# Kernel tuning notes

Measured on AMD Instinct MI355X. Metric: run time of the kernel, lower is better.

The kernel has to match this reference:

```python
import jax, jax.numpy as jnp
import numpy as np

B, C, H, W = 2, 64, 256, 256
SIZE, STRIDE = 8, 4
NUMS = (H - SIZE) // STRIDE + 1          # 63 patches per axis
L = NUMS * NUMS                           # 3969 patches
K2 = SIZE * SIZE                          # 64 pixels per patch
EPS = 1e-05
TABLE = (2 * NUMS - 1) * (2 * NUMS - 1)   # relative-position bias table size


def _unfold_idx():
    # linear pixel index for each (kernel-offset k, patch l): [K2, L]
    i0 = np.arange(NUMS) * STRIDE
    j0 = np.arange(NUMS) * STRIDE
    kh = np.arange(SIZE)
    kw = np.arange(SIZE)
    r = kh[:, None, None, None] + i0[None, None, :, None]   # [S,1,N,1]
    c = kw[None, :, None, None] + j0[None, None, None, :]   # [1,S,1,N]
    return (r * W + c).reshape(K2, L)


def _rel_pos_index():
    ch = np.arange(NUMS)
    cw = np.arange(NUMS)
    coords = np.stack(np.meshgrid(ch, cw, indexing='ij'))   # [2,N,N]
    cf = coords.reshape(2, -1)                               # [2,L]
    rc = (cf[:, :, None] - cf[:, None, :]).transpose(1, 2, 0).astype(np.int64)
    rc[:, :, 0] += NUMS - 1
    rc[:, :, 1] += NUMS - 1
    rc[:, :, 0] *= 2 * NUMS - 1
    return rc.sum(-1)                                        # [L,L]


_IDX_NP = _unfold_idx()
_IDX = jnp.asarray(_IDX_NP)
_RPI = jnp.asarray(_rel_pos_index())
_count_np = np.zeros(H * W, np.float32)
np.add.at(_count_np, _IDX_NP.ravel(), 1.0)
_COUNT = jnp.asarray(_count_np.reshape(1, 1, H, W))


def setup_inputs() -> dict:
    key = jax.random.key(0)
    ks = jax.random.split(key, 9)
    x = jax.random.normal(ks[0], (B, C, H, W), dtype=jnp.float32)
    mask = jnp.round(jax.random.uniform(ks[1], (B, 1, H, W), dtype=jnp.float32))
    fg_gamma = 0.1 * jax.random.normal(ks[2], (C,), dtype=jnp.float32)
    fg_beta = 0.1 * jax.random.normal(ks[3], (C,), dtype=jnp.float32)
    bg_gamma = 0.1 * jax.random.normal(ks[4], (C,), dtype=jnp.float32)
    bg_beta = 0.1 * jax.random.normal(ks[5], (C,), dtype=jnp.float32)
    w_fore = 0.02 * jax.random.normal(ks[6], (C, C, K2), dtype=jnp.float32)
    w_back = 0.02 * jax.random.normal(ks[7], (C, C, K2), dtype=jnp.float32)
    rpb_table = 0.02 * jax.random.normal(ks[8], (TABLE,), dtype=jnp.float32)
    return {"x": x, "mask": mask, "fg_gamma": fg_gamma, "fg_beta": fg_beta,
            "bg_gamma": bg_gamma, "bg_beta": bg_beta,
            "w_fore": w_fore, "w_back": w_back, "rpb_table": rpb_table}


def _unfold(t):
    # [B,Ct,H,W] -> [B,Ct,L,K2]  (gather patch pixels)
    b, ct = t.shape[0], t.shape[1]
    return t.reshape(b, ct, H * W)[:, :, _IDX].transpose(0, 1, 3, 2)


def _patch_mean_std(region, m):
    # region [B,Ct,L,K2], m [B,1,L,K2] -> mu, 'std' (actually variance, per source)
    num = m.sum(-1)                                   # [B,1,L]
    mu = region.sum(-1) / (num + EPS)                 # [B,Ct,L]
    var = ((region - m * mu[..., None]) ** 2).sum(-1) / (num + EPS)
    return mu, var


def reference(x, mask, fg_gamma, fg_beta, bg_gamma, bg_beta, w_fore, w_back, rpb_table):
    # mask is already HxW -> nearest interpolate is identity
    invm = 1.0 - mask
    background = x * invm
    foreground = x * mask
    unorm_bg = (background * (1.0 + bg_gamma[None, :, None, None])
                + bg_beta[None, :, None, None]) * invm

    pb = _unfold(background)          # [B,C,L,K2]
    pf = _unfold(foreground)
    pm = _unfold(mask)                # [B,1,L,K2]

    mb, sb = _patch_mean_std(pb, 1.0 - pm)
    mf, sf = _patch_mean_std(pf, pm)

    in_b = (pb - mb[..., None]) / sb[..., None] * (1.0 - pm) + mb[..., None] * pm
    in_f = (pf - mf[..., None]) / sf[..., None] * pm + mf[..., None] * (1.0 - pm)

    tok_b = jnp.einsum('bclk,dck->bdl', in_b, w_back)   # [B,C,L]
    tok_f = jnp.einsum('bclk,dck->bdl', in_f, w_fore)

    bias = rpb_table[_RPI.reshape(-1)].reshape(L, L)
    S = jax.nn.softmax(jnp.einsum('bcl,bcm->blm', tok_f, tok_b) + bias[None], axis=-1)

    new_std = jnp.einsum('blm,bcm->bcl', S, sb)[..., None]   # [B,C,L,1]
    new_pf = in_f * new_std + new_std                        # (source uses new_std twice)

    # fold: scatter-add overlapping patches back, divide by coverage count
    flat = new_pf.transpose(0, 1, 3, 2).reshape(B, C, K2 * L)
    folded = jnp.zeros((B, C, H * W), x.dtype).at[:, :, _IDX.reshape(-1)].add(flat)
    new_fg = folded.reshape(B, C, H, W) / _COUNT

    new_fg = (new_fg * (1.0 + fg_gamma[None, :, None, None])
              + fg_beta[None, :, None, None]) * mask
    return new_fg + unorm_bg
```

## Files before the change

kernel.cpp:

```cpp
#include <hip/hip_runtime.h>
#include <stdint.h>

#define L_   3969
#define LP   3972
#define EPS_ 1e-5f
#define LOG2E 1.4426950408889634f
#define MH   6
#define IMR  11
#define PLANE 254208

#define OFF_MF   0
#define OFF_SF   508416
#define OFF_MB   1016832
#define OFF_SB   1525248
#define OFF_TOKF 2033664
#define OFF_TOKB 2542080
#define OFF_PACC 3050496
#define OFF_PM   6100992
#define OFF_PD   6148656
#define OFF_WT   6196320
#define PART_SLICE 1016832

#define OFF_A    2033664
#define OFF_B    2542080
#define OFF_C    4067328

typedef __attribute__((ext_vector_type(8))) short bf16x8;
typedef __attribute__((ext_vector_type(4))) float f32x4;

__device__ __forceinline__ uint16_t bf16_rne(float f) {
    uint32_t u = __float_as_uint(f);
    return (uint16_t)((u + 0x7FFFu + ((u >> 16) & 1u)) >> 16);
}
__device__ __forceinline__ void split_bf16(float v, uint16_t& h, uint16_t& l) {
    uint32_t u = __float_as_uint(v);
    uint32_t hu = u & 0xFFFF0000u;
    h = (uint16_t)(hu >> 16);
    l = bf16_rne(v - __uint_as_float(hu));
}
__device__ __forceinline__ uint4 pack8(const uint16_t* s) {
    uint4 r;
    r.x = (uint32_t)s[0] | ((uint32_t)s[1] << 16);
    r.y = (uint32_t)s[2] | ((uint32_t)s[3] << 16);
    r.z = (uint32_t)s[4] | ((uint32_t)s[5] << 16);
    r.w = (uint32_t)s[6] | ((uint32_t)s[7] << 16);
    return r;
}
__device__ __forceinline__ uint32_t pkhi2(float a, float b) {
    return (__float_as_uint(a) >> 16) | (__float_as_uint(b) & 0xFFFF0000u);
}
__device__ __forceinline__ uint32_t pklo2(float a, float b) {
    float ra = a - __uint_as_float(__float_as_uint(a) & 0xFFFF0000u);
    float rb = b - __uint_as_float(__float_as_uint(b) & 0xFFFF0000u);
    uint32_t r;
    asm("v_cvt_pk_bf16_f32 %0, %1, %2" : "=v"(r) : "v"(ra), "v"(rb));
    return r;
}

__global__ void k0_w2(const float* __restrict__ wf, const float* __restrict__ wb,
                      float* __restrict__ ws) {
    int c = blockIdx.x, t = blockIdx.y;
    const float* w = t ? wb : wf;
    uint16_t* w2 = (uint16_t*)(ws + OFF_WT);
    int tid = threadIdx.x;
    int lane = tid & 63, dq = tid >> 6;
    int d = dq * 16 + (lane & 15), quad = lane >> 4;
    for (int kci = 0; kci < 2; ++kci) {
        int k = kci * 32 + quad * 8;
        const float* src = w + (size_t)(d * 64 + c) * 64 + k;
        uint16_t hb[8], lb[8];
#pragma unroll
        for (int j = 0; j < 8; ++j) split_bf16(src[j], hb[j], lb[j]);
        size_t base = ((size_t)(((t * 64 + c) * 2 + kci) * 4 + dq) * 2) * 512 + lane * 8;
        *(uint4*)(w2 + base) = pack8(hb);
        *(uint4*)(w2 + base + 512) = pack8(lb);
    }
}

__global__ void k1_stats(const float* __restrict__ x, const float* __restrict__ mask,
                         float* __restrict__ ws) {
    int i = blockIdx.x, c = blockIdx.y, b = blockIdx.z;
    __shared__ float xs[8 * 256];
    __shared__ float ms[8 * 256];
    __shared__ float pS[5][256];
    int t = threadIdx.x;
    const float* xr = x + (((b * 64 + c) * 256) + i * 4) * 256;
    const float* mr = mask + (b * 256 + i * 4) * 256;
#pragma unroll
    for (int r = 0; r < 8; ++r) {
        xs[r * 256 + t] = xr[r * 256 + t];
        ms[r * 256 + t] = mr[r * 256 + t];
    }
    __syncthreads();
    int q = t >> 6, j = t & 63;
    float Sa = 0, Qa = 0, Sf = 0, Qf = 0, Nf = 0;
    if (j < 63) {
#pragma unroll
        for (int rr = 0; rr < 2; ++rr) {
            int base = (q * 2 + rr) * 256 + j * 4;
#pragma unroll
            for (int cc = 0; cc < 8; ++cc) {
                float v = xs[base + cc], m = ms[base + cc];
                Sa += v; Qa += v * v; Sf += v * m; Qf += v * v * m; Nf += m;
            }
        }
    }
    pS[0][t] = Sa; pS[1][t] = Qa; pS[2][t] = Sf; pS[3][t] = Qf; pS[4][t] = Nf;
    __syncthreads();
    if (q == 0 && j < 63) {
        Sa = pS[0][j] + pS[0][j + 64] + pS[0][j + 128] + pS[0][j + 192];
        Qa = pS[1][j] + pS[1][j + 64] + pS[1][j + 128] + pS[1][j + 192];
        Sf = pS[2][j] + pS[2][j + 64] + pS[2][j + 128] + pS[2][j + 192];
        Qf = pS[3][j] + pS[3][j + 64] + pS[3][j + 128] + pS[3][j + 192];
        Nf = pS[4][j] + pS[4][j + 64] + pS[4][j + 128] + pS[4][j + 192];
        float nb = 64.0f - Nf;
        float muf = Sf / (Nf + EPS_);
        float vaf = (Qf - 2.f * muf * Sf + Nf * muf * muf) / (Nf + EPS_);
        float Sb = Sa - Sf, Qb = Qa - Qf;
        float mub = Sb / (nb + EPS_);
        float vab = (Qb - 2.f * mub * Sb + nb * mub * mub) / (nb + EPS_);
        int idx = (b * 64 + c) * LP + i * 63 + j;
        ws[OFF_MF + idx] = muf; ws[OFF_SF + idx] = vaf;
        ws[OFF_MB + idx] = mub; ws[OFF_SB + idx] = vab;
    }
}

__global__ __launch_bounds__(256)
void k2_tok(const float* __restrict__ x, const float* __restrict__ mask,
            const float* __restrict__ wsc, float* __restrict__ ws) {
    int il = blockIdx.x, kc = blockIdx.y, b = blockIdx.z;
    int tid = threadIdx.x;
    int jl = tid & 63;
    int q = tid >> 6;
    __shared__ uint16_t IN[2][4 * 64 * 72];
    const uint16_t* w2 = (const uint16_t*)(wsc + OFF_WT);

    bool lv = jl < 63;
    int lg = il * 63 + jl;

    uint32_t mbits[2] = {0u, 0u};
    if (lv) {
#pragma unroll
        for (int oi = 0; oi < 2; ++oi) {
            int o = q + oi * 4;
            const float* mp = mask + (size_t)b * 65536 + (il * 4 + o) * 256 + jl * 4;
            float4 m0 = *(const float4*)mp;
            float4 m1 = *(const float4*)(mp + 4);
            uint32_t bits = 0;
            bits |= (m0.x != 0.f) ? 1u : 0u;  bits |= (m0.y != 0.f) ? 2u : 0u;
            bits |= (m0.z != 0.f) ? 4u : 0u;  bits |= (m0.w != 0.f) ? 8u : 0u;
            bits |= (m1.x != 0.f) ? 16u : 0u; bits |= (m1.y != 0.f) ? 32u : 0u;
            bits |= (m1.z != 0.f) ? 64u : 0u; bits |= (m1.w != 0.f) ? 128u : 0u;
            mbits[oi] = bits;
        }
    }

    f32x4 acc[2][2][2];
#pragma unroll
    for (int t = 0; t < 2; ++t)
#pragma unroll
        for (int i2 = 0; i2 < 2; ++i2)
#pragma unroll
            for (int j2 = 0; j2 < 2; ++j2) acc[t][i2][j2] = (f32x4)(0.f);

    int lane = tid & 63;
    int quad = lane >> 4;
    int c16 = lane & 15;
    int wd = q >> 1, wl = q & 1;
    int c0 = kc * 16;

    float4 xa[2][2];
    if (!lv) {
        xa[0][0] = xa[0][1] = xa[1][0] = xa[1][1] = make_float4(0.f, 0.f, 0.f, 0.f);
    }
    float muF = 0.f, vaF = 1.f, muB = 0.f, vaB = 1.f;

#define K2_LOADCH(cc)                                                                \
    do {                                                                             \
        if (lv) {                                                                    \
            int si = (b * 64 + (cc)) * LP + lg;                                      \
            muF = wsc[OFF_MF + si]; vaF = wsc[OFF_SF + si];                          \
            muB = wsc[OFF_MB + si]; vaB = wsc[OFF_SB + si];                          \
            const float* xp0 = x + (size_t)(b * 64 + (cc)) * 65536 + (il * 4 + q) * 256 + jl * 4; \
            xa[0][0] = *(const float4*)xp0;                                          \
            xa[0][1] = *(const float4*)(xp0 + 4);                                    \
            xa[1][0] = *(const float4*)(xp0 + 1024);                                 \
            xa[1][1] = *(const float4*)(xp0 + 1028);                                 \
        }                                                                            \
    } while (0)

#define K2_PACKSTORE(bufsel)                                                         \
    do {                                                                             \
        float invF = lv ? (1.0f / vaF) : 0.f;                                        \
        float invB = lv ? (1.0f / vaB) : 0.f;                                        \
        float cmF = lv ? muF : 0.f;                                                  \
        float cmB = lv ? muB : 0.f;                                                  \
        _Pragma("unroll")                                                            \
        for (int oi = 0; oi < 2; ++oi) {                                             \
            float xv[8];                                                             \
            xv[0] = xa[oi][0].x; xv[1] = xa[oi][0].y;                                \
            xv[2] = xa[oi][0].z; xv[3] = xa[oi][0].w;                                \
            xv[4] = xa[oi][1].x; xv[5] = xa[oi][1].y;                                \
            xv[6] = xa[oi][1].z; xv[7] = xa[oi][1].w;                                \
            float fv[8], bv[8];                                                      \
            _Pragma("unroll")                                                        \
            for (int j = 0; j < 8; ++j) {                                            \
                bool mf = (mbits[oi] >> j) & 1;                                      \
                float v = xv[j];                                                     \
                fv[j] = mf ? (v - cmF) * invF : cmF;                                 \
                bv[j] = mf ? cmB : (v - cmB) * invB;                                 \
            }                                                                        \
            uint4 FH, FL, BH, BL;                                                    \
            FH.x = pkhi2(fv[0], fv[1]); FH.y = pkhi2(fv[2], fv[3]);                  \
            FH.z = pkhi2(fv[4], fv[5]); FH.w = pkhi2(fv[6], fv[7]);                  \
            FL.x = pklo2(fv[0], fv[1]); FL.y = pklo2(fv[2], fv[3]);                  \
            FL.z = pklo2(fv[4], fv[5]); FL.w = pklo2(fv[6], fv[7]);                  \
            BH.x = pkhi2(bv[0], bv[1]); BH.y = pkhi2(bv[2], bv[3]);                  \
            BH.z = pkhi2(bv[4], bv[5]); BH.w = pkhi2(bv[6], bv[7]);                  \
            BL.x = pklo2(bv[0], bv[1]); BL.y = pklo2(bv[2], bv[3]);                  \
            BL.z = pklo2(bv[4], bv[5]); BL.w = pklo2(bv[6], bv[7]);                  \
            uint16_t* dst = &IN[bufsel][jl * 72 + (q + oi * 4) * 8];                 \
            *(uint4*)(dst)         = FH;                                             \
            *(uint4*)(dst + 4608)  = FL;                                             \
            *(uint4*)(dst + 9216)  = BH;                                             \
            *(uint4*)(dst + 13824) = BL;                                             \
        }                                                                            \
    } while (0)

#define K2_MFMA(bufi, cch)                                                           \
    do {                                                                             \
        _Pragma("unroll")                                                            \
        for (int t = 0; t < 2; ++t) {                                                \
            _Pragma("unroll")                                                        \
            for (int kci = 0; kci < 2; ++kci) {                                      \
                bf16x8 Ah[2], Al[2];                                                 \
                _Pragma("unroll")                                                    \
                for (int dqi = 0; dqi < 2; ++dqi) {                                  \
                    const uint16_t* ab = w2 +                                        \
                        ((size_t)(((t * 64 + (cch)) * 2 + kci) * 4 + (wd * 2 + dqi)) * 2) * 512 + lane * 8; \
                    Ah[dqi] = *(const bf16x8*)ab;                                    \
                    Al[dqi] = *(const bf16x8*)(ab + 512);                            \
                }                                                                    \
                _Pragma("unroll")                                                    \
                for (int lt = 0; lt < 2; ++lt) {                                     \
                    const uint16_t* bp = &IN[bufi][(t * 2) * 4608 +                  \
                        (wl * 32 + lt * 16 + c16) * 72 + kci * 32 + quad * 8];       \
                    bf16x8 Bh = *(const bf16x8*)bp;                                  \
                    bf16x8 Bl = *(const bf16x8*)(bp + 4608);                         \
                    _Pragma("unroll")                                                \
                    for (int dqi = 0; dqi < 2; ++dqi) {                              \
                        acc[t][dqi][lt] = __builtin_amdgcn_mfma_f32_16x16x32_bf16(Ah[dqi], Bh, acc[t][dqi][lt], 0, 0, 0); \
                        acc[t][dqi][lt] = __builtin_amdgcn_mfma_f32_16x16x32_bf16(Ah[dqi], Bl, acc[t][dqi][lt], 0, 0, 0); \
                        acc[t][dqi][lt] = __builtin_amdgcn_mfma_f32_16x16x32_bf16(Al[dqi], Bh, acc[t][dqi][lt], 0, 0, 0); \
                    }                                                                \
                }                                                                    \
            }                                                                        \
        }                                                                            \
    } while (0)

    K2_LOADCH(c0);
    K2_PACKSTORE(0);
    K2_LOADCH(c0 + 1);
    __syncthreads();

#pragma unroll 2
    for (int ci = 0; ci < 16; ++ci) {
        int cur = ci & 1;
        if (ci < 15) {
            K2_PACKSTORE(cur ^ 1);
            if (ci < 14) K2_LOADCH(c0 + ci + 2);
        }
        K2_MFMA(cur, c0 + ci);
        __syncthreads();
    }
#undef K2_LOADCH
#undef K2_PACKSTORE
#undef K2_MFMA

    float* ST = (float*)&IN[0][0];
#pragma unroll
    for (int t = 0; t < 2; ++t) {
        __syncthreads();
#pragma unroll
        for (int dqi = 0; dqi < 2; ++dqi)
#pragma unroll
            for (int lt = 0; lt < 2; ++lt)
#pragma unroll
                for (int r = 0; r < 4; ++r)
                    ST[(wl * 32 + lt * 16 + c16) * 68 + (wd * 2 + dqi) * 16 + quad * 4 + r] =
                        acc[t][dqi][lt][r];
        __syncthreads();
        float* dst = ws + OFF_TOKF + (size_t)kc * PART_SLICE + ((t * 2 + b) * (size_t)LP) * 64;
        int d4 = (tid & 15) * 4;
#pragma unroll
        for (int pass = 0; pass < 4; ++pass) {
            int l = pass * 16 + (tid >> 4);
            if (l < 63)
                *(float4*)&dst[(size_t)(il * 63 + l) * 64 + d4] = *(float4*)&ST[l * 68 + d4];
        }
    }
}

__global__ void k2r_reduce(float* __restrict__ ws) {
    size_t e = ((size_t)blockIdx.x * 256 + threadIdx.x) * 4;
    float4 a0 = *(float4*)&ws[OFF_TOKF + e];
    float4 a1 = *(float4*)&ws[OFF_TOKF + PART_SLICE + e];
    float4 a2 = *(float4*)&ws[OFF_TOKF + 2 * PART_SLICE + e];
    float4 a3 = *(float4*)&ws[OFF_TOKF + 3 * PART_SLICE + e];
    float s0 = a0.x + a1.x + a2.x + a3.x;
    float s1 = a0.y + a1.y + a2.y + a3.y;
    float s2 = a0.z + a1.z + a2.z + a3.z;
    float s3 = a0.w + a1.w + a2.w + a3.w;
    int tb = (int)(e / (size_t)PLANE);
    int idx = (int)(e - (size_t)tb * PLANE);
    int t = tb >> 1, b = tb & 1;
    uint16_t* pl = (uint16_t*)(ws + (t ? OFF_WT : OFF_SB));
    uint2 hv, lv;
    hv.x = pkhi2(s0, s1); hv.y = pkhi2(s2, s3);
    lv.x = pklo2(s0, s1); lv.y = pklo2(s2, s3);
    *(uint2*)&pl[(size_t)(b * 2 + 0) * PLANE + idx] = hv;
    *(uint2*)&pl[(size_t)(b * 2 + 1) * PLANE + idx] = lv;
}

__global__ void k1s_sb(float* __restrict__ ws) {
    int im = blockIdx.x, b = blockIdx.y;
    int tid = threadIdx.x;
    int c = tid >> 2, mm = (tid & 3) * 16;
    const float* src = ws + OFF_SB + ((size_t)b * 64 + c) * LP + im * 63 + mm;
    uint16_t sv[16];
#pragma unroll
    for (int u = 0; u < 16; ++u)
        sv[u] = (mm + u < 63) ? bf16_rne(src[u]) : (uint16_t)0;
    uint16_t* dst = (uint16_t*)(ws + OFF_MB) + (((size_t)b * 63 + im) * 64 + c) * 64 + mm;
    *(uint4*)(dst) = pack8(sv);
    *(uint4*)(dst + 8) = pack8(sv + 8);
}

__global__ __launch_bounds__(256, 4)
void k3_attn(const float* __restrict__ wsc, const float* __restrict__ rpb,
             float* __restrict__ ws) {
    int il = blockIdx.x, imc = blockIdx.y, b = blockIdx.z;
    int tid = threadIdx.x;
    int w = tid >> 6, lane = tid & 63;
    int c16 = lane & 15, quad = lane >> 4;

    __shared__ uint16_t TBh[64 * 72];
    __shared__ uint16_t TBl[64 * 72];
    __shared__ uint16_t SB[64 * 72];
    __shared__ uint16_t P[64 * 72];
    __shared__ float bias_r[128];

    const uint16_t* tfp = (const uint16_t*)(wsc + OFF_SB);
    const uint16_t* tbp = (const uint16_t*)(wsc + OFF_WT);
    const uint16_t* TFH = tfp + (size_t)(b * 2 + 0) * PLANE;
    const uint16_t* TFL = tfp + (size_t)(b * 2 + 1) * PLANE;
    const uint16_t* TBH = tbp + (size_t)(b * 2 + 0) * PLANE;
    const uint16_t* TBL = tbp + (size_t)(b * 2 + 1) * PLANE;
    const uint16_t* sbb = (const uint16_t*)(wsc + OFF_MB);

    int qrow = il * 63 + w * 16 + c16;
    bf16x8 Qh[2], Ql[2];
#pragma unroll
    for (int kk = 0; kk < 2; ++kk) {
        Qh[kk] = *(const bf16x8*)&TFH[(size_t)qrow * 64 + kk * 32 + quad * 8];
        Ql[kk] = *(const bf16x8*)&TFL[(size_t)qrow * 64 + kk * 32 + quad * 8];
    }

    float mrun = -1e30f, drun = 0.f;
    f32x4 acc2[4];
#pragma unroll
    for (int ct = 0; ct < 4; ++ct) acc2[ct] = (f32x4)(0.f);

    int im0 = imc * IMR;
    int im1 = min(63, im0 + IMR);

    int jms = tid >> 2, ccs = (tid & 3) * 16;
    uint4 rTH0, rTH1, rTL0, rTL1, rS0, rS1;
    float rBias;

#define K3_PREFETCH(imv)                                                              \
    do {                                                                              \
        if (jms < 63) {                                                               \
            const uint16_t* sh_ = TBH + (size_t)((imv) * 63 + jms) * 64 + ccs;        \
            const uint16_t* sl_ = TBL + (size_t)((imv) * 63 + jms) * 64 + ccs;        \
            rTH0 = *(const uint4*)sh_; rTH1 = *(const uint4*)(sh_ + 8);               \
            rTL0 = *(const uint4*)sl_; rTL1 = *(const uint4*)(sl_ + 8);               \
        } else {                                                                      \
            rTH0 = rTH1 = rTL0 = rTL1 = make_uint4(0u,0u,0u,0u);                      \
        }                                                                             \
        const uint16_t* ss_ = sbb + (((size_t)b * 63 + (imv)) * 64 + jms) * 64 + ccs; \
        rS0 = *(const uint4*)ss_; rS1 = *(const uint4*)(ss_ + 8);                     \
        rBias = (tid < 125) ? rpb[(il - (imv) + 62) * 125 + tid] : 0.f;               \
    } while (0)

    K3_PREFETCH(im0);

    int ibias = w * 16 + c16 + 62 - quad * 4;

    for (int im = im0; im < im1; ++im) {
        __syncthreads();
        *(uint4*)&TBh[jms * 72 + ccs] = rTH0; *(uint4*)&TBh[jms * 72 + ccs + 8] = rTH1;
        *(uint4*)&TBl[jms * 72 + ccs] = rTL0; *(uint4*)&TBl[jms * 72 + ccs + 8] = rTL1;
        *(uint4*)&SB[jms * 72 + ccs]  = rS0;  *(uint4*)&SB[jms * 72 + ccs + 8]  = rS1;
        if (tid < 128) bias_r[tid] = rBias;
        if (im + 1 < im1) K3_PREFETCH(im + 1);
        __syncthreads();

        f32x4 Z[4];
#pragma unroll
        for (int jt = 0; jt < 4; ++jt) Z[jt] = (f32x4)(0.f);
#pragma unroll
        for (int jt = 0; jt < 4; ++jt) {
#pragma unroll
            for (int kk = 0; kk < 2; ++kk) {
                bf16x8 Kh = *(bf16x8*)&TBh[(jt * 16 + c16) * 72 + kk * 32 + quad * 8];
                bf16x8 Kl = *(bf16x8*)&TBl[(jt * 16 + c16) * 72 + kk * 32 + quad * 8];
                Z[jt] = __builtin_amdgcn_mfma_f32_16x16x32_bf16(Kh, Qh[kk], Z[jt], 0, 0, 0);
                Z[jt] = __builtin_amdgcn_mfma_f32_16x16x32_bf16(Kh, Ql[kk], Z[jt], 0, 0, 0);
                Z[jt] = __builtin_amdgcn_mfma_f32_16x16x32_bf16(Kl, Qh[kk], Z[jt], 0, 0, 0);
            }
        }

        float zv[4][4];
#pragma unroll
        for (int jt = 0; jt < 4; ++jt)
#pragma unroll
            for (int r = 0; r < 4; ++r) {
                int m = jt * 16 + quad * 4 + r;
                int bi = ibias - jt * 16 - r;
                bi = bi < 0 ? 0 : bi;
                zv[jt][r] = (m == 63) ? -1e30f : (Z[jt][r] + bias_r[bi]);
            }

        float a0 = fmaxf(zv[0][0], zv[0][1]), a1 = fmaxf(zv[0][2], zv[0][3]);
        float a2 = fmaxf(zv[1][0], zv[1][1]), a3 = fmaxf(zv[1][2], zv[1][3]);
        float a4 = fmaxf(zv[2][0], zv[2][1]), a5 = fmaxf(zv[2][2], zv[2][3]);
        float a6 = fmaxf(zv[3][0], zv[3][1]), a7 = fmaxf(zv[3][2], zv[3][3]);
        a0 = fmaxf(a0, a1); a2 = fmaxf(a2, a3); a4 = fmaxf(a4, a5); a6 = fmaxf(a6, a7);
        float vmax = fmaxf(fmaxf(a0, a2), fmaxf(a4, a6));
        vmax = fmaxf(vmax, __shfl_xor(vmax, 16));
        vmax = fmaxf(vmax, __shfl_xor(vmax, 32));
        float mnew = fmaxf(mrun, vmax);
        float alpha = exp2f((mrun - mnew) * LOG2E);
        uint16_t pb[4][4];
        float sv[8];
#pragma unroll
        for (int jt = 0; jt < 4; ++jt) {
            float p0 = exp2f((zv[jt][0] - mnew) * LOG2E);
            float p1 = exp2f((zv[jt][1] - mnew) * LOG2E);
            float p2 = exp2f((zv[jt][2] - mnew) * LOG2E);
            float p3 = exp2f((zv[jt][3] - mnew) * LOG2E);
            uint16_t h0 = bf16_rne(p0), h1 = bf16_rne(p1);
            uint16_t h2 = bf16_rne(p2), h3 = bf16_rne(p3);
            pb[jt][0] = h0; pb[jt][1] = h1; pb[jt][2] = h2; pb[jt][3] = h3;
            sv[jt * 2]     = __uint_as_float((uint32_t)h0 << 16) + __uint_as_float((uint32_t)h1 << 16);
            sv[jt * 2 + 1] = __uint_as_float((uint32_t)h2 << 16) + __uint_as_float((uint32_t)h3 << 16);
        }
        float s = ((sv[0] + sv[1]) + (sv[2] + sv[3])) + ((sv[4] + sv[5]) + (sv[6] + sv[7]));
        s += __shfl_xor(s, 16);
        s += __shfl_xor(s, 32);
        drun = drun * alpha + s;
        mrun = mnew;

        float alphav[4];
#pragma unroll
        for (int r = 0; r < 4; ++r) alphav[r] = __shfl(alpha, quad * 4 + r, 16);
#pragma unroll
        for (int ct = 0; ct < 4; ++ct)
#pragma unroll
            for (int r = 0; r < 4; ++r) acc2[ct][r] *= alphav[r];

#pragma unroll
        for (int jt = 0; jt < 4; ++jt) {
            uint2 pw;
            pw.x = (uint32_t)pb[jt][0] | ((uint32_t)pb[jt][1] << 16);
            pw.y = (uint32_t)pb[jt][2] | ((uint32_t)pb[jt][3] << 16);
            *(uint2*)&P[(w * 16 + c16) * 72 + jt * 16 + quad * 4] = pw;
        }
        asm volatile("" ::: "memory");

#pragma unroll
        for (int kk = 0; kk < 2; ++kk) {
            bf16x8 Pf = *(bf16x8*)&P[(w * 16 + c16) * 72 + kk * 32 + quad * 8];
#pragma unroll
            for (int ct = 0; ct < 4; ++ct) {
                bf16x8 Sf = *(bf16x8*)&SB[(ct * 16 + c16) * 72 + kk * 32 + quad * 8];
                acc2[ct] = __builtin_amdgcn_mfma_f32_16x16x32_bf16(Pf, Sf, acc2[ct], 0, 0, 0);
            }
        }
        asm volatile("" ::: "memory");
    }

    float* PA = ws + OFF_PACC + ((imc * 2 + b) * (size_t)LP) * 64;
#pragma unroll
    for (int r = 0; r < 4; ++r) {
        int i = w * 16 + quad * 4 + r;
        if (i < 63) {
            int rl = il * 63 + i;
#pragma unroll
            for (int ct = 0; ct < 4; ++ct)
                PA[(size_t)rl * 64 + ct * 16 + c16] = acc2[ct][r];
        }
    }
    if (quad == 0) {
        int i = w * 16 + c16;
        if (i < 63) {
            int rl = il * 63 + i;
            ws[OFF_PM + (imc * 2 + b) * LP + rl] = mrun;
            ws[OFF_PD + (imc * 2 + b) * LP + rl] = drun;
        }
    }
#undef K3_PREFETCH
}

__global__ void k3b_merge(float* __restrict__ ws) {
    int b = blockIdx.y;
    int l = blockIdx.x * 4 + (threadIdx.x >> 6);
    int c = threadIdx.x & 63;
    if (l >= L_) return;
    float M = -1e30f;
#pragma unroll
    for (int p = 0; p < MH; ++p)
        M = fmaxf(M, ws[OFF_PM + (p * 2 + b) * LP + l]);
    float denom = 0.f, num = 0.f;
#pragma unroll
    for (int p = 0; p < MH; ++p) {
        float w = exp2f((ws[OFF_PM + (p * 2 + b) * LP + l] - M) * LOG2E);
        denom += ws[OFF_PD + (p * 2 + b) * LP + l] * w;
        num += ws[OFF_PACC + ((p * 2 + b) * (size_t)LP + l) * 64 + c] * w;
    }
    ws[OFF_PACC + (b * (size_t)LP + l) * 64 + c] = num / denom;
}

__global__ void k3c_coef(float* __restrict__ ws) {
    int b = blockIdx.y;
    int bl = blockIdx.x;
    int tid = threadIdx.x;
    __shared__ float T[3][4][65];
    int ls = tid >> 6, c = tid & 63;
    int l = bl * 4 + ls;
    float ns = ws[OFF_PACC + ((size_t)b * LP + l) * 64 + c];
    float mf = ws[OFF_MF + (size_t)(b * 64 + c) * LP + l];
    float sf = ws[OFF_SF + (size_t)(b * 64 + c) * LP + l];
    float a = ns / sf;
    T[0][ls][c] = a;
    T[1][ls][c] = ns - mf * a;
    T[2][ls][c] = ns * (mf + 1.f);
    __syncthreads();
    int c2 = tid >> 2, l2 = tid & 3;
    size_t o = (size_t)(b * 64 + c2) * LP + bl * 4 + l2;
    ws[OFF_A + o] = T[0][l2][c2];
    ws[OFF_B + o] = T[1][l2][c2];
    ws[OFF_C + o] = T[2][l2][c2];
}

__global__ void k4_fold(const float* __restrict__ x, const float* __restrict__ mask,
                        const float* __restrict__ fg_g, const float* __restrict__ fg_b,
                        const float* __restrict__ bg_g, const float* __restrict__ bg_b,
                        const float* __restrict__ wsc, float* __restrict__ out) {
    int gid = blockIdx.x * 256 + threadIdx.x;
    int col = gid & 255, r = (gid >> 8) & 255, c = (gid >> 16) & 63, b = gid >> 22;
    float xv = x[gid];
    float m = mask[b * 65536 + r * 256 + col];
    int imin = (r >= 4) ? ((r - 4) >> 2) : 0;
    int imax = min(62, r >> 2);
    int jmin = (col >= 4) ? ((col - 4) >> 2) : 0;
    int jmax = min(62, col >> 2);
    bool fi = imax > imin, fj = jmax > jmin;
    int l00 = imin * 63 + jmin;
    const float* Aa = wsc + OFF_A + (size_t)(b * 64 + c) * LP;
    const float* Ba = wsc + OFF_B + (size_t)(b * 64 + c) * LP;
    const float* Ca = wsc + OFF_C + (size_t)(b * 64 + c) * LP;
    float a00 = Aa[l00],      b00 = Ba[l00],      c00 = Ca[l00];
    float a01 = Aa[l00 + 1],  b01 = Ba[l00 + 1],  c01 = Ca[l00 + 1];
    float a10 = Aa[l00 + 63], b10 = Ba[l00 + 63], c10 = Ca[l00 + 63];
    float a11 = Aa[l00 + 64], b11 = Ba[l00 + 64], c11 = Ca[l00 + 64];
    bool fij = fi && fj;
    float SA = a00 + (fj ? a01 : 0.f) + (fi ? a10 : 0.f) + (fij ? a11 : 0.f);
    float SBv = b00 + (fj ? b01 : 0.f) + (fi ? b10 : 0.f) + (fij ? b11 : 0.f);
    float SCv = c00 + (fj ? c01 : 0.f) + (fi ? c10 : 0.f) + (fij ? c11 : 0.f);
    float folded = (m != 0.f) ? (xv * SA + SBv) : SCv;
    float rc = (fi ? 0.5f : 1.f) * (fj ? 0.5f : 1.f);
    float invm = 1.f - m;
    float ub = (xv * invm * (1.f + bg_g[c]) + bg_b[c]) * invm;
    float nf = (folded * rc * (1.f + fg_g[c]) + fg_b[c]) * m;
    out[gid] = nf + ub;
}

extern "C" void kernel_launch(void* const* d_in, const int* in_sizes, int n_in,
                              void* d_out, int out_size, void* d_ws, size_t ws_size,
                              hipStream_t stream) {
    const float* x    = (const float*)d_in[0];
    const float* mask = (const float*)d_in[1];
    const float* fg_g = (const float*)d_in[2];
    const float* fg_b = (const float*)d_in[3];
    const float* bg_g = (const float*)d_in[4];
    const float* bg_b = (const float*)d_in[5];
    const float* wf   = (const float*)d_in[6];
    const float* wb   = (const float*)d_in[7];
    const float* rpb  = (const float*)d_in[8];
    float* ws = (float*)d_ws;
    float* out = (float*)d_out;

    k0_w2<<<dim3(64, 2), 256, 0, stream>>>(wf, wb, ws);
    k1_stats<<<dim3(63, 64, 2), 256, 0, stream>>>(x, mask, ws);
    k2_tok<<<dim3(63, 4, 2), 256, 0, stream>>>(x, mask, ws, ws);
    k1s_sb<<<dim3(63, 2), 256, 0, stream>>>(ws);
    k2r_reduce<<<dim3(993), 256, 0, stream>>>(ws);
    k3_attn<<<dim3(63, MH, 2), 256, 0, stream>>>(ws, rpb, ws);
    k3b_merge<<<dim3(993, 2), 256, 0, stream>>>(ws);
    k3c_coef<<<dim3(993, 2), 256, 0, stream>>>(ws);
    k4_fold<<<dim3(32768), 256, 0, stream>>>(x, mask, fg_g, fg_b, bg_g, bg_b, ws, out);
}
```

Measured before the change: 246.1 us.

## Halve k2_tok LDS by staging fore/back tiles alternately, raise occupancy

```diff
diff --git a/kernel.cpp b/kernel.cpp
--- a/kernel.cpp
+++ b/kernel.cpp
@@ -47,7 +47,7 @@
     return r;
 }
 __device__ __forceinline__ uint32_t pkhi2(float a, float b) {
-    return (__float_as_uint(a) >> 16) | (__float_as_uint(b) & 0xFFFF0000u);
+    return __builtin_amdgcn_perm(__float_as_uint(b), __float_as_uint(a), 0x07060302u);
 }
 __device__ __forceinline__ uint32_t pklo2(float a, float b) {
     float ra = a - __uint_as_float(__float_as_uint(a) & 0xFFFF0000u);
@@ -125,14 +125,14 @@
     }
 }
 
-__global__ __launch_bounds__(256)
+__global__ __launch_bounds__(256, 4)
 void k2_tok(const float* __restrict__ x, const float* __restrict__ mask,
             const float* __restrict__ wsc, float* __restrict__ ws) {
     int il = blockIdx.x, kc = blockIdx.y, b = blockIdx.z;
     int tid = threadIdx.x;
     int jl = tid & 63;
     int q = tid >> 6;
-    __shared__ uint16_t IN[2][4 * 64 * 72];
+    __shared__ uint16_t IN[2][2 * 64 * 72];
     const uint16_t* w2 = (const uint16_t*)(wsc + OFF_WT);
 
     bool lv = jl < 63;
@@ -169,113 +169,111 @@
     int wd = q >> 1, wl = q & 1;
     int c0 = kc * 16;
 
-    float4 xa[2][2];
+    float4 xa[2][2][2];
+    float muF[2] = {0.f, 0.f}, vaF[2] = {1.f, 1.f};
+    float muB[2] = {0.f, 0.f}, vaB[2] = {1.f, 1.f};
     if (!lv) {
-        xa[0][0] = xa[0][1] = xa[1][0] = xa[1][1] = make_float4(0.f, 0.f, 0.f, 0.f);
-    }
-    float muF = 0.f, vaF = 1.f, muB = 0.f, vaB = 1.f;
-
-#define K2_LOADCH(cc)                                                                \
+#pragma unroll
+        for (int sl = 0; sl < 2; ++sl)
+#pragma unroll
+            for (int oi = 0; oi < 2; ++oi)
+#pragma unroll
+                for (int hf = 0; hf < 2; ++hf)
+                    xa[sl][oi][hf] = make_float4(0.f, 0.f, 0.f, 0.f);
+    }
+
+#define K2_LOADCH(sl, cc)                                                            \
     do {                                                                             \
         if (lv) {                                                                    \
             int si = (b * 64 + (cc)) * LP + lg;                                      \
-            muF = wsc[OFF_MF + si]; vaF = wsc[OFF_SF + si];                          \
-            muB = wsc[OFF_MB + si]; vaB = wsc[OFF_SB + si];                          \
+            muF[sl] = wsc[OFF_MF + si]; vaF[sl] = wsc[OFF_SF + si];                  \
+            muB[sl] = wsc[OFF_MB + si]; vaB[sl] = wsc[OFF_SB + si];                  \
             const float* xp0 = x + (size_t)(b * 64 + (cc)) * 65536 + (il * 4 + q) * 256 + jl * 4; \
-            xa[0][0] = *(const float4*)xp0;                                          \
-            xa[0][1] = *(const float4*)(xp0 + 4);                                    \
-            xa[1][0] = *(const float4*)(xp0 + 1024);                                 \
-            xa[1][1] = *(const float4*)(xp0 + 1028);                                 \
+            xa[sl][0][0] = *(const float4*)xp0;                                      \
+            xa[sl][0][1] = *(const float4*)(xp0 + 4);                                \
+            xa[sl][1][0] = *(const float4*)(xp0 + 1024);                             \
+            xa[sl][1][1] = *(const float4*)(xp0 + 1028);                             \
         }                                                                            \
     } while (0)
 
-#define K2_PACKSTORE(bufsel)                                                         \
+#define K2_PACKT(ts, sl)                                                             \
     do {                                                                             \
-        float invF = lv ? (1.0f / vaF) : 0.f;                                        \
-        float invB = lv ? (1.0f / vaB) : 0.f;                                        \
-        float cmF = lv ? muF : 0.f;                                                  \
-        float cmB = lv ? muB : 0.f;                                                  \
+        float va_ = (ts) ? vaB[sl] : vaF[sl];                                        \
+        float mu_ = (ts) ? muB[sl] : muF[sl];                                        \
+        float inv_ = lv ? (1.0f / va_) : 0.f;                                        \
+        float cm_ = lv ? mu_ : 0.f;                                                  \
         _Pragma("unroll")                                                            \
         for (int oi = 0; oi < 2; ++oi) {                                             \
             float xv[8];                                                             \
-            xv[0] = xa[oi][0].x; xv[1] = xa[oi][0].y;                                \
-            xv[2] = xa[oi][0].z; xv[3] = xa[oi][0].w;                                \
-            xv[4] = xa[oi][1].x; xv[5] = xa[oi][1].y;                                \
-            xv[6] = xa[oi][1].z; xv[7] = xa[oi][1].w;                                \
-            float fv[8], bv[8];                                                      \
+            xv[0] = xa[sl][oi][0].x; xv[1] = xa[sl][oi][0].y;                        \
+            xv[2] = xa[sl][oi][0].z; xv[3] = xa[sl][oi][0].w;                        \
+            xv[4] = xa[sl][oi][1].x; xv[5] = xa[sl][oi][1].y;                        \
+            xv[6] = xa[sl][oi][1].z; xv[7] = xa[sl][oi][1].w;                        \
+            float fv[8];                                                             \
             _Pragma("unroll")                                                        \
             for (int j = 0; j < 8; ++j) {                                            \
                 bool mf = (mbits[oi] >> j) & 1;                                      \
                 float v = xv[j];                                                     \
-                fv[j] = mf ? (v - cmF) * invF : cmF;                                 \
-                bv[j] = mf ? cmB : (v - cmB) * invB;                                 \
+                float nrm = (v - cm_) * inv_;                                        \
+                fv[j] = (ts) ? (mf ? cm_ : nrm) : (mf ? nrm : cm_);                  \
             }                                                                        \
-            uint4 FH, FL, BH, BL;                                                    \
-            FH.x = pkhi2(fv[0], fv[1]); FH.y = pkhi2(fv[2], fv[3]);                  \
-            FH.z = pkhi2(fv[4], fv[5]); FH.w = pkhi2(fv[6], fv[7]);                  \
-            FL.x = pklo2(fv[0], fv[1]); FL.y = pklo2(fv[2], fv[3]);                  \
-            FL.z = pklo2(fv[4], fv[5]); FL.w = pklo2(fv[6], fv[7]);                  \
-            BH.x = pkhi2(bv[0], bv[1]); BH.y = pkhi2(bv[2], bv[3]);                  \
-            BH.z = pkhi2(bv[4], bv[5]); BH.w = pkhi2(bv[6], bv[7]);                  \
-            BL.x = pklo2(bv[0], bv[1]); BL.y = pklo2(bv[2], bv[3]);                  \
-            BL.z = pklo2(bv[4], bv[5]); BL.w = pklo2(bv[6], bv[7]);                  \
-            uint16_t* dst = &IN[bufsel][jl * 72 + (q + oi * 4) * 8];                 \
-            *(uint4*)(dst)         = FH;                                             \
-            *(uint4*)(dst + 4608)  = FL;                                             \
-            *(uint4*)(dst + 9216)  = BH;                                             \
-            *(uint4*)(dst + 13824) = BL;                                             \
+            uint4 H, L;                                                              \
+            H.x = pkhi2(fv[0], fv[1]); H.y = pkhi2(fv[2], fv[3]);                    \
+            H.z = pkhi2(fv[4], fv[5]); H.w = pkhi2(fv[6], fv[7]);                    \
+            L.x = pklo2(fv[0], fv[1]); L.y = pklo2(fv[2], fv[3]);                    \
+            L.z = pklo2(fv[4], fv[5]); L.w = pklo2(fv[6], fv[7]);                    \
+            uint16_t* dst = &IN[ts][jl * 72 + (q + oi * 4) * 8];                     \
+            *(uint4*)(dst)        = H;                                               \
+            *(uint4*)(dst + 4608) = L;                                               \
         }                                                                            \
     } while (0)
 
-#define K2_MFMA(bufi, cch)                                                           \
+#define K2_MFMAT(ts, cch)                                                            \
     do {                                                                             \
         _Pragma("unroll")                                                            \
-        for (int t = 0; t < 2; ++t) {                                                \
+        for (int kci = 0; kci < 2; ++kci) {                                          \
+            bf16x8 Ah[2], Al[2];                                                     \
             _Pragma("unroll")                                                        \
-            for (int kci = 0; kci < 2; ++kci) {                                      \
-                bf16x8 Ah[2], Al[2];                                                 \
+            for (int dqi = 0; dqi < 2; ++dqi) {                                      \
+                const uint16_t* ab = w2 +                                            \
+                    ((size_t)((((ts) * 64 + (cch)) * 2 + kci) * 4 + (wd * 2 + dqi)) * 2) * 512 + lane * 8; \
+                Ah[dqi] = *(const bf16x8*)ab;                                        \
+                Al[dqi] = *(const bf16x8*)(ab + 512);                                \
+            }                                                                        \
+            _Pragma("unroll")                                                        \
+            for (int lt = 0; lt < 2; ++lt) {                                         \
+                const uint16_t* bp = &IN[ts][(wl * 32 + lt * 16 + c16) * 72 + kci * 32 + quad * 8]; \
+                bf16x8 Bh = *(const bf16x8*)bp;                                      \
+                bf16x8 Bl = *(const bf16x8*)(bp + 4608);                             \
                 _Pragma("unroll")                                                    \
                 for (int dqi = 0; dqi < 2; ++dqi) {                                  \
-                    const uint16_t* ab = w2 +                                        \
-                        ((size_t)(((t * 64 + (cch)) * 2 + kci) * 4 + (wd * 2 + dqi)) * 2) * 512 + lane * 8; \
-                    Ah[dqi] = *(const bf16x8*)ab;                                    \
-                    Al[dqi] = *(const bf16x8*)(ab + 512);                            \
-                }                                                                    \
-                _Pragma("unroll")                                                    \
-                for (int lt = 0; lt < 2; ++lt) {                                     \
-                    const uint16_t* bp = &IN[bufi][(t * 2) * 4608 +                  \
-                        (wl * 32 + lt * 16 + c16) * 72 + kci * 32 + quad * 8];       \
-                    bf16x8 Bh = *(const bf16x8*)bp;                                  \
-                    bf16x8 Bl = *(const bf16x8*)(bp + 4608);                         \
-                    _Pragma("unroll")                                                \
-                    for (int dqi = 0; dqi < 2; ++dqi) {                              \
-                        acc[t][dqi][lt] = __builtin_amdgcn_mfma_f32_16x16x32_bf16(Ah[dqi], Bh, acc[t][dqi][lt], 0, 0, 0); \
-                        acc[t][dqi][lt] = __builtin_amdgcn_mfma_f32_16x16x32_bf16(Ah[dqi], Bl, acc[t][dqi][lt], 0, 0, 0); \
-                        acc[t][dqi][lt] = __builtin_amdgcn_mfma_f32_16x16x32_bf16(Al[dqi], Bh, acc[t][dqi][lt], 0, 0, 0); \
-                    }                                                                \
+                    acc[ts][dqi][lt] = __builtin_amdgcn_mfma_f32_16x16x32_bf16(Ah[dqi], Bh, acc[ts][dqi][lt], 0, 0, 0); \
+                    acc[ts][dqi][lt] = __builtin_amdgcn_mfma_f32_16x16x32_bf16(Ah[dqi], Bl, acc[ts][dqi][lt], 0, 0, 0); \
+                    acc[ts][dqi][lt] = __builtin_amdgcn_mfma_f32_16x16x32_bf16(Al[dqi], Bh, acc[ts][dqi][lt], 0, 0, 0); \
                 }                                                                    \
             }                                                                        \
         }                                                                            \
     } while (0)
 
-    K2_LOADCH(c0);
-    K2_PACKSTORE(0);
-    K2_LOADCH(c0 + 1);
+    K2_LOADCH(0, c0);
+    K2_PACKT(0, 0);
+    K2_LOADCH(1, c0 + 1);
     __syncthreads();
 
 #pragma unroll 2
     for (int ci = 0; ci < 16; ++ci) {
-        int cur = ci & 1;
-        if (ci < 15) {
-            K2_PACKSTORE(cur ^ 1);
-            if (ci < 14) K2_LOADCH(c0 + ci + 2);
-        }
-        K2_MFMA(cur, c0 + ci);
+        int sl = ci & 1;
+        K2_PACKT(1, sl);
+        if (ci < 14) K2_LOADCH(sl, c0 + ci + 2);
+        K2_MFMAT(0, c0 + ci);
         __syncthreads();
+        if (ci < 15) K2_PACKT(0, sl ^ 1);
+        K2_MFMAT(1, c0 + ci);
+        __syncthreads();
     }
 #undef K2_LOADCH
-#undef K2_PACKSTORE
-#undef K2_MFMA
+#undef K2_PACKT
+#undef K2_MFMAT
 
     float* ST = (float*)&IN[0][0];
 #pragma unroll
```

Result: slower. 257.1 us (+4.4%).
